# Optimization experiments

Measured on AMD Instinct MI355X. Metric: run time of the kernel, lower is better.

## Reference

```python
import jax, jax.numpy as jnp
import numpy as np

jax.config.update("jax_enable_x64", True)  # torch casts to double for matrix_exp

EPS_DIAG = 1e-6


def setup_inputs() -> dict:
    key = jax.random.key(0)
    B, D, NB, S = 32, 128, 8, 128
    ks = jax.random.split(key, 9)
    return {
        "z0r": jax.random.normal(ks[0], (B, D), jnp.float32),
        "z0i": jax.random.normal(ks[1], (B, D), jnp.float32),
        # uniform grid: dt = time_steps[0] = 0.01, diffs == dt (uniform branch)
        "time_steps": (jnp.arange(S, dtype=jnp.float32) + 1.0) * 0.01,
        "k_coeffs": jax.random.normal(ks[2], (B, NB), jnp.float32),
        "r_coeffs": jax.random.normal(ks[3], (B, NB), jnp.float32),
        "alpha": jax.random.normal(ks[4], (B, 1), jnp.float32),
        "beta": jax.random.normal(ks[5], (B, 1), jnp.float32),
        "K_bases": jax.random.normal(ks[6], (NB, D, D), jnp.float32) * 0.01,
        "R_bases": jax.random.normal(ks[7], (NB, D, D), jnp.float32) * 0.01,
    }


def _build_generator(k_coeffs, r_coeffs, alpha, beta, K_bases, R_bases):
    # A = alpha * skew(K_sum) + beta * -(R_sum^T @ R_sum), per batch element
    K_sum = jnp.einsum("bn,nij->bij", k_coeffs, K_bases)
    R_sum = jnp.einsum("bn,nij->bij", r_coeffs, R_bases)
    skew = K_sum - jnp.swapaxes(K_sum, -1, -2)
    neg_gram = -jnp.einsum("bji,bjk->bik", R_sum, R_sum)  # -(R^T @ R)
    return alpha[..., None] * skew + beta[..., None] * neg_gram  # (B, D, D)


def _propagators(A, time_steps, uniform):
    D = A.shape[-1]
    S = time_steps.shape[0]
    if uniform:
        dt = time_steps[0]
        A64 = A.astype(jnp.float64) * dt.astype(jnp.float64) + EPS_DIAG * jnp.eye(D, dtype=jnp.float64)
        M = jax.vmap(jax.scipy.linalg.expm)(A64).astype(jnp.complex64)  # (B, D, D)
        # cumulative matrix powers M, M^2, ..., M^S via O(log S) associative scan
        Ms = jnp.broadcast_to(M[:, None], (M.shape[0], S, D, D))
        props = jax.lax.associative_scan(jnp.matmul, Ms, axis=1)
    else:
        A_t = A[:, None].astype(jnp.float64) * time_steps.astype(jnp.float64)[None, :, None, None]
        props = jax.vmap(jax.vmap(jax.scipy.linalg.expm))(A_t).astype(jnp.complex64)
    return props  # (B, S, D, D)


def reference(z0r, z0i, time_steps, k_coeffs, r_coeffs, alpha, beta, K_bases, R_bases):
    ts = np.asarray(time_steps)
    uniform = ts.shape[0] <= 1 or np.allclose(ts[1:] - ts[:-1], ts[0], atol=1e-6)
    A = _build_generator(k_coeffs, r_coeffs, alpha, beta, K_bases, R_bases)
    props = _propagators(A, time_steps, uniform)
    z = (z0r + 1j * z0i).astype(jnp.complex64)  # (B, D)
    # z_evolved[b, s, o] = sum_i z[b, i] * props[b, s, o, i]
    return jnp.einsum("bi,bsoi->bso", z, props)
```

## Files before the change

### kernel.cpp

```cpp
#include <hip/hip_runtime.h>

#define BATCH   32
#define DIM     128
#define NBASES  8
#define SSTEPS  128
#define LDA     136

typedef __attribute__((ext_vector_type(8))) short s8v;
typedef __attribute__((ext_vector_type(4))) short s4v;
typedef __attribute__((ext_vector_type(4))) float f4v;

__device__ __forceinline__ f4v mf(s8v a, s8v b, f4v c) {
    return __builtin_amdgcn_mfma_f32_16x16x32_bf16(a, b, c, 0, 0, 0);
}
__device__ __forceinline__ s8v ld8(const short* p) {
    return *reinterpret_cast<const s8v*>(p);
}
__device__ __forceinline__ void st4(short* p, s4v v) {
    *reinterpret_cast<s4v*>(p) = v;
}
__device__ __forceinline__ float upbf(short h) {
    return __uint_as_float(((unsigned)(unsigned short)h) << 16);
}
__device__ __forceinline__ void splitbf(float v, short& hi, short& lo) {
    const unsigned u = __float_as_uint(v);
    hi = (short)(u >> 16);
    const float fh = __uint_as_float(u & 0xffff0000u);
    lo = (short)(__float_as_uint(v - fh) >> 16);
}

__device__ __forceinline__ void write_out(float* __restrict__ outF, int b, int sidx,
                                          int o, int c, float val,
                                          int interleaved, int out_size)
{
    if (interleaved) {
        const int oi = ((b * SSTEPS + sidx) * DIM + o) * 2 + c;
        if (oi < out_size) outF[oi] = val;
    } else if (c == 0) {
        const int oi = (b * SSTEPS + sidx) * DIM + o;
        if (oi < out_size) outF[oi] = val;
    }
}

__device__ __forceinline__ void mm_full(const short* __restrict__ Ah,
                                        const short* __restrict__ Al,
                                        const short* __restrict__ Bh,
                                        const short* __restrict__ Bl,
                                        f4v acc[2][4], int w, int lane)
{
    const int l15 = lane & 15, quad = lane >> 4;
    const int mb = (w & 3) * 32, nb = (w >> 2) * 64;
    #pragma unroll
    for (int kk = 0; kk < DIM; kk += 32) {
        const int ko = kk + quad * 8;
        const s8v a0h = ld8(Ah + (mb +      l15) * LDA + ko);
        const s8v a0l = ld8(Al + (mb +      l15) * LDA + ko);
        const s8v a1h = ld8(Ah + (mb + 16 + l15) * LDA + ko);
        const s8v a1l = ld8(Al + (mb + 16 + l15) * LDA + ko);
        #pragma unroll
        for (int ni = 0; ni < 4; ++ni) {
            const s8v bh = ld8(Bh + (nb + ni * 16 + l15) * LDA + ko);
            const s8v bl = ld8(Bl + (nb + ni * 16 + l15) * LDA + ko);
            acc[0][ni] = mf(a0h, bh, acc[0][ni]);
            acc[0][ni] = mf(a0h, bl, acc[0][ni]);
            acc[0][ni] = mf(a0l, bh, acc[0][ni]);
            acc[1][ni] = mf(a1h, bh, acc[1][ni]);
            acc[1][ni] = mf(a1h, bl, acc[1][ni]);
            acc[1][ni] = mf(a1l, bh, acc[1][ni]);
        }
    }
}

__global__ __launch_bounds__(512, 1)
void htg_mfma(const float* __restrict__ z0r, const float* __restrict__ z0i,
              const float* __restrict__ ts,  const float* __restrict__ kco,
              const float* __restrict__ rco, const float* __restrict__ alp,
              const float* __restrict__ bet, const float* __restrict__ KB,
              const float* __restrict__ RB,  float* __restrict__ outF,
              int interleaved, int out_size)
{
    __shared__ short nm_hi[DIM * LDA], nm_lo[DIM * LDA];
    __shared__ short tr_hi[DIM * LDA], tr_lo[DIM * LDA];
    __shared__ short ht_hi[32 * LDA],  ht_lo[32 * LDA];

    const int b = blockIdx.x, t = threadIdx.x;
    const int w = t >> 6, lane = t & 63;
    const int l15 = lane & 15, quad = lane >> 4;
    const f4v z4 = {0.f, 0.f, 0.f, 0.f};
    const int mb = (w & 3) * 32, nb = (w >> 2) * 64;

    {
        float rc[NBASES], kc[NBASES];
        #pragma unroll
        for (int n = 0; n < NBASES; ++n) {
            rc[n] = rco[b * NBASES + n];
            kc[n] = kco[b * NBASES + n];
        }
        #pragma unroll
        for (int q = 0; q < 8; ++q) {
            const int e = q * 2048 + t * 4;
            float4 r4 = {0.f, 0.f, 0.f, 0.f}, k4 = {0.f, 0.f, 0.f, 0.f};
            #pragma unroll
            for (int n = 0; n < NBASES; ++n) {
                const float4 rv = *reinterpret_cast<const float4*>(RB + n * DIM * DIM + e);
                const float4 kv = *reinterpret_cast<const float4*>(KB + n * DIM * DIM + e);
                r4.x += rc[n] * rv.x; r4.y += rc[n] * rv.y;
                r4.z += rc[n] * rv.z; r4.w += rc[n] * rv.w;
                k4.x += kc[n] * kv.x; k4.y += kc[n] * kv.y;
                k4.z += kc[n] * kv.z; k4.w += kc[n] * kv.w;
            }
            const int r = e >> 7, c = e & 127;
            const float rr[4] = {r4.x, r4.y, r4.z, r4.w};
            const float kk[4] = {k4.x, k4.y, k4.z, k4.w};
            s4v kh, kl;
            #pragma unroll
            for (int j = 0; j < 4; ++j) {
                short hi, lo;
                splitbf(rr[j], hi, lo);
                tr_hi[(c + j) * LDA + r] = hi; tr_lo[(c + j) * LDA + r] = lo;
                splitbf(kk[j], hi, lo);
                kh[j] = hi; kl[j] = lo;
            }
            st4(&nm_hi[r * LDA + c], kh);
            st4(&nm_lo[r * LDA + c], kl);
        }
        if (t < 2 * DIM) {
            const int c = t >> 7, o = t & 127;
            const float zv = (c == 0) ? z0r[b * DIM + o] : z0i[b * DIM + o];
            short hi, lo; splitbf(zv, hi, lo);
            ht_hi[c * LDA + o] = hi; ht_lo[c * LDA + o] = lo;
        }
    }
    __syncthreads();

    f4v acc[2][4];

    #pragma unroll
    for (int i = 0; i < 2; ++i)
        #pragma unroll
        for (int j = 0; j < 4; ++j) acc[i][j] = z4;
    mm_full(tr_hi, tr_lo, tr_hi, tr_lo, acc, w, lane);
    __syncthreads();
    {
        const float alpha = alp[b], beta = bet[b], dtf = ts[0];
        #pragma unroll
        for (int mi = 0; mi < 2; ++mi)
            #pragma unroll
            for (int ni = 0; ni < 4; ++ni)
                #pragma unroll
                for (int r = 0; r < 4; ++r) {
                    const int row = mb + mi * 16 + quad * 4 + r;
                    const int col = nb + ni * 16 + l15;
                    const float k1 = upbf(nm_hi[row * LDA + col]) + upbf(nm_lo[row * LDA + col]);
                    const float k2 = upbf(nm_hi[col * LDA + row]) + upbf(nm_lo[col * LDA + row]);
                    float x = (alpha * (k1 - k2) - beta * acc[mi][ni][r]) * dtf;
                    if (row == col) x += 1e-6f;
                    acc[mi][ni][r] = x;
                }
    }
    __syncthreads();
    #pragma unroll
    for (int mi = 0; mi < 2; ++mi)
        #pragma unroll
        for (int ni = 0; ni < 4; ++ni) {
            const int row0 = mb + mi * 16 + quad * 4;
            const int col  = nb + ni * 16 + l15;
            s4v h4, l4;
            #pragma unroll
            for (int r = 0; r < 4; ++r) {
                short hi, lo;
                splitbf(acc[mi][ni][r], hi, lo);
                nm_hi[(row0 + r) * LDA + col] = hi;
                nm_lo[(row0 + r) * LDA + col] = lo;
                h4[r] = hi; l4[r] = lo;
            }
            st4(&tr_hi[col * LDA + row0], h4);
            st4(&tr_lo[col * LDA + row0], l4);
        }
    __syncthreads();

    float a1v[2][4][4];
    #pragma unroll
    for (int i = 0; i < 2; ++i)
        #pragma unroll
        for (int j = 0; j < 4; ++j) acc[i][j] = z4;
    mm_full(nm_hi, nm_lo, tr_hi, tr_lo, acc, w, lane);
    __syncthreads();
    #pragma unroll
    for (int mi = 0; mi < 2; ++mi)
        #pragma unroll
        for (int ni = 0; ni < 4; ++ni) {
            const int row0 = mb + mi * 16 + quad * 4;
            const int col  = nb + ni * 16 + l15;
            s4v h4, l4;
            #pragma unroll
            for (int r = 0; r < 4; ++r) {
                const int row = row0 + r;
                const float xv = upbf(nm_hi[row * LDA + col]) + upbf(nm_lo[row * LDA + col]);
                const float cv = acc[mi][ni][r];
                a1v[mi][ni][r] = ((row == col) ? 1.f : 0.f) + xv + 0.5f * cv;
                const float a2 = xv * (1.f / 6.f) + cv * (1.f / 24.f);
                short hi, lo;
                splitbf(cv, hi, lo);
                nm_hi[row * LDA + col] = hi;
                nm_lo[row * LDA + col] = lo;
                splitbf(a2, hi, lo);
                h4[r] = hi; l4[r] = lo;
            }
            st4(&tr_hi[col * LDA + row0], h4);
            st4(&tr_lo[col * LDA + row0], l4);
        }
    __syncthreads();

    #pragma unroll
    for (int mi = 0; mi < 2; ++mi)
        #pragma unroll
        for (int ni = 0; ni < 4; ++ni)
            #pragma unroll
            for (int r = 0; r < 4; ++r) acc[mi][ni][r] = a1v[mi][ni][r];
    mm_full(nm_hi, nm_lo, tr_hi, tr_lo, acc, w, lane);
    __syncthreads();
    #pragma unroll
    for (int mi = 0; mi < 2; ++mi)
        #pragma unroll
        for (int ni = 0; ni < 4; ++ni) {
            const int row0 = mb + mi * 16 + quad * 4;
            const int col  = nb + ni * 16 + l15;
            s4v h4, l4;
            #pragma unroll
            for (int r = 0; r < 4; ++r) {
                short hi, lo;
                splitbf(acc[mi][ni][r], hi, lo);
                nm_hi[(row0 + r) * LDA + col] = hi;
                nm_lo[(row0 + r) * LDA + col] = lo;
                h4[r] = hi; l4[r] = lo;
            }
            st4(&tr_hi[col * LDA + row0], h4);
            st4(&tr_lo[col * LDA + row0], l4);
        }
    __syncthreads();

    #pragma unroll
    for (int stage = 0; stage < 4; ++stage) {
        const int J = 1 << stage;
        f4v ar = z4;
        #pragma unroll
        for (int i = 0; i < 2; ++i)
            #pragma unroll
            for (int j = 0; j < 4; ++j) acc[i][j] = z4;
        #pragma unroll
        for (int kk = 0; kk < DIM; kk += 32) {
            const int ko = kk + quad * 8;
            const s8v rah = ld8(nm_hi + (w * 16 + l15) * LDA + ko);
            const s8v ral = ld8(nm_lo + (w * 16 + l15) * LDA + ko);
            const s8v rbh = ld8(ht_hi + l15 * LDA + ko);
            const s8v rbl = ld8(ht_lo + l15 * LDA + ko);
            ar = mf(rah, rbh, ar);
            ar = mf(rah, rbl, ar);
            ar = mf(ral, rbh, ar);
        }
        mm_full(nm_hi, nm_lo, tr_hi, tr_lo, acc, w, lane);
        __syncthreads();
        if (l15 < 2 * J) {
            const int o0 = w * 16 + quad * 4;
            const int sidx = (l15 >> 1) + J - 1;
            s4v h4, l4;
            #pragma unroll
            for (int r = 0; r < 4; ++r) {
                short hi, lo;
                splitbf(ar[r], hi, lo);
                h4[r] = hi; l4[r] = lo;
                write_out(outF, b, sidx, o0 + r, l15 & 1, ar[r], interleaved, out_size);
            }
            st4(&ht_hi[(l15 + 2 * J) * LDA + o0], h4);
            st4(&ht_lo[(l15 + 2 * J) * LDA + o0], l4);
        }
        #pragma unroll
        for (int mi = 0; mi < 2; ++mi)
            #pragma unroll
            for (int ni = 0; ni < 4; ++ni) {
                const int row0 = mb + mi * 16 + quad * 4;
                const int col  = nb + ni * 16 + l15;
                s4v h4, l4;
                #pragma unroll
                for (int r = 0; r < 4; ++r) {
                    short hi, lo;
                    splitbf(acc[mi][ni][r], hi, lo);
                    nm_hi[(row0 + r) * LDA + col] = hi;
                    nm_lo[(row0 + r) * LDA + col] = lo;
                    h4[r] = hi; l4[r] = lo;
                }
                st4(&tr_hi[col * LDA + row0], h4);
                st4(&tr_lo[col * LDA + row0], l4);
            }
        __syncthreads();
    }

    s8v vah[4], val[4];
    #pragma unroll
    for (int k4 = 0; k4 < 4; ++k4) {
        const int ko = k4 * 32 + quad * 8;
        vah[k4] = ld8(nm_hi + (w * 16 + l15) * LDA + ko);
        val[k4] = ld8(nm_lo + (w * 16 + l15) * LDA + ko);
    }
    for (int q = 1; q <= 7; ++q) {
        f4v a2[2] = {z4, z4};
        #pragma unroll
        for (int k4 = 0; k4 < 4; ++k4) {
            const int ko = k4 * 32 + quad * 8;
            #pragma unroll
            for (int ci = 0; ci < 2; ++ci) {
                const s8v bh = ld8(ht_hi + (ci * 16 + l15) * LDA + ko);
                const s8v bl = ld8(ht_lo + (ci * 16 + l15) * LDA + ko);
                a2[ci] = mf(vah[k4], bh, a2[ci]);
                a2[ci] = mf(vah[k4], bl, a2[ci]);
                a2[ci] = mf(val[k4], bh, a2[ci]);
            }
        }
        __syncthreads();
        const int o0 = w * 16 + quad * 4;
        #pragma unroll
        for (int ci = 0; ci < 2; ++ci) {
            const int n = ci * 16 + l15;
            const int sidx = 16 * q + (n >> 1) - 1;
            s4v h4, l4;
            #pragma unroll
            for (int r = 0; r < 4; ++r) {
                short hi, lo;
                splitbf(a2[ci][r], hi, lo);
                h4[r] = hi; l4[r] = lo;
                write_out(outF, b, sidx, o0 + r, n & 1, a2[ci][r], interleaved, out_size);
            }
            if (q < 7 || n < 2) {
                st4(&ht_hi[n * LDA + o0], h4);
                st4(&ht_lo[n * LDA + o0], l4);
            }
        }
        __syncthreads();
    }

    if (t < 2 * DIM) {
        const int c = t >> 7, o = t & 127;
        float a = 0.f;
        #pragma unroll 4
        for (int i = 0; i < DIM; ++i)
            a += (upbf(tr_hi[i * LDA + o]) + upbf(tr_lo[i * LDA + o]))
               * (upbf(ht_hi[c * LDA + i]) + upbf(ht_lo[c * LDA + i]));
        write_out(outF, b, 127, o, c, a, interleaved, out_size);
    }
}

extern "C" void kernel_launch(void* const* d_in, const int* in_sizes, int n_in,
                              void* d_out, int out_size, void* d_ws, size_t ws_size,
                              hipStream_t stream)
{
    (void)in_sizes; (void)n_in; (void)d_ws; (void)ws_size;
    const float* z0r = (const float*)d_in[0];
    const float* z0i = (const float*)d_in[1];
    const float* ts  = (const float*)d_in[2];
    const float* kco = (const float*)d_in[3];
    const float* rco = (const float*)d_in[4];
    const float* alp = (const float*)d_in[5];
    const float* bet = (const float*)d_in[6];
    const float* KB  = (const float*)d_in[7];
    const float* RB  = (const float*)d_in[8];
    float* outF = (float*)d_out;

    const int interleaved = (out_size >= 2 * BATCH * SSTEPS * DIM) ? 1 : 0;

    htg_mfma<<<dim3(BATCH), dim3(512), 0, stream>>>(
        z0r, z0i, ts, kco, rco, alp, bet, KB, RB, outF, interleaved, out_size);
}
```

Before: 122.4 us.

## Double threads per block to 1024 and split matmul tiles across 16 waves

The block grows from 8 to 16 waves. Each wave's 128x128 matmul tile shrinks from 32x64 to 32x32, the z-propagation MFMA stage splits its output columns across wave pairs, and the final dot product is split four ways with a shared-memory reduction. The goal is more latency hiding and more MFMA issue parallelism inside each CU, since only 32 blocks run on a GPU with many more CUs. The cost is that the A-fragment loads are now duplicated across more waves. Barriers also involve more waves, and register pressure is tighter under the 1024-thread launch bound.

```diff
diff --git a/kernel.cpp b/kernel.cpp
--- a/kernel.cpp
+++ b/kernel.cpp
@@ -46,10 +46,9 @@
                                         const short* __restrict__ Al,
                                         const short* __restrict__ Bh,
                                         const short* __restrict__ Bl,
-                                        f4v acc[2][4], int w, int lane)
+                                        f4v acc[2][2], int mb, int nb, int lane)
 {
     const int l15 = lane & 15, quad = lane >> 4;
-    const int mb = (w & 3) * 32, nb = (w >> 2) * 64;
     #pragma unroll
     for (int kk = 0; kk < DIM; kk += 32) {
         const int ko = kk + quad * 8;
@@ -58,7 +57,7 @@
         const s8v a1h = ld8(Ah + (mb + 16 + l15) * LDA + ko);
         const s8v a1l = ld8(Al + (mb + 16 + l15) * LDA + ko);
         #pragma unroll
-        for (int ni = 0; ni < 4; ++ni) {
+        for (int ni = 0; ni < 2; ++ni) {
             const s8v bh = ld8(Bh + (nb + ni * 16 + l15) * LDA + ko);
             const s8v bl = ld8(Bl + (nb + ni * 16 + l15) * LDA + ko);
             acc[0][ni] = mf(a0h, bh, acc[0][ni]);
@@ -71,7 +70,7 @@
     }
 }
 
-__global__ __launch_bounds__(512, 1)
+__global__ __launch_bounds__(1024, 1)
 void htg_mfma(const float* __restrict__ z0r, const float* __restrict__ z0i,
               const float* __restrict__ ts,  const float* __restrict__ kco,
               const float* __restrict__ rco, const float* __restrict__ alp,
@@ -82,12 +81,13 @@
     __shared__ short nm_hi[DIM * LDA], nm_lo[DIM * LDA];
     __shared__ short tr_hi[DIM * LDA], tr_lo[DIM * LDA];
     __shared__ short ht_hi[32 * LDA],  ht_lo[32 * LDA];
+    __shared__ float s_part[1024];
 
     const int b = blockIdx.x, t = threadIdx.x;
     const int w = t >> 6, lane = t & 63;
     const int l15 = lane & 15, quad = lane >> 4;
     const f4v z4 = {0.f, 0.f, 0.f, 0.f};
-    const int mb = (w & 3) * 32, nb = (w >> 2) * 64;
+    const int mb = (w & 3) * 32, nb = (w >> 2) * 32;
 
     {
         float rc[NBASES], kc[NBASES];
@@ -97,8 +97,8 @@
             kc[n] = kco[b * NBASES + n];
         }
         #pragma unroll
-        for (int q = 0; q < 8; ++q) {
-            const int e = q * 2048 + t * 4;
+        for (int q = 0; q < 4; ++q) {
+            const int e = q * 4096 + t * 4;
             float4 r4 = {0.f, 0.f, 0.f, 0.f}, k4 = {0.f, 0.f, 0.f, 0.f};
             #pragma unroll
             for (int n = 0; n < NBASES; ++n) {
@@ -133,20 +133,20 @@
     }
     __syncthreads();
 
-    f4v acc[2][4];
+    f4v acc[2][2];
 
     #pragma unroll
     for (int i = 0; i < 2; ++i)
         #pragma unroll
-        for (int j = 0; j < 4; ++j) acc[i][j] = z4;
-    mm_full(tr_hi, tr_lo, tr_hi, tr_lo, acc, w, lane);
+        for (int j = 0; j < 2; ++j) acc[i][j] = z4;
+    mm_full(tr_hi, tr_lo, tr_hi, tr_lo, acc, mb, nb, lane);
     __syncthreads();
     {
         const float alpha = alp[b], beta = bet[b], dtf = ts[0];
         #pragma unroll
         for (int mi = 0; mi < 2; ++mi)
             #pragma unroll
-            for (int ni = 0; ni < 4; ++ni)
+            for (int ni = 0; ni < 2; ++ni)
                 #pragma unroll
                 for (int r = 0; r < 4; ++r) {
                     const int row = mb + mi * 16 + quad * 4 + r;
@@ -162,7 +162,7 @@
     #pragma unroll
     for (int mi = 0; mi < 2; ++mi)
         #pragma unroll
-        for (int ni = 0; ni < 4; ++ni) {
+        for (int ni = 0; ni < 2; ++ni) {
             const int row0 = mb + mi * 16 + quad * 4;
             const int col  = nb + ni * 16 + l15;
             s4v h4, l4;
@@ -179,17 +179,17 @@
         }
     __syncthreads();
 
-    float a1v[2][4][4];
+    float a1v[2][2][4];
     #pragma unroll
     for (int i = 0; i < 2; ++i)
         #pragma unroll
-        for (int j = 0; j < 4; ++j) acc[i][j] = z4;
-    mm_full(nm_hi, nm_lo, tr_hi, tr_lo, acc, w, lane);
+        for (int j = 0; j < 2; ++j) acc[i][j] = z4;
+    mm_full(nm_hi, nm_lo, tr_hi, tr_lo, acc, mb, nb, lane);
     __syncthreads();
     #pragma unroll
     for (int mi = 0; mi < 2; ++mi)
         #pragma unroll
-        for (int ni = 0; ni < 4; ++ni) {
+        for (int ni = 0; ni < 2; ++ni) {
             const int row0 = mb + mi * 16 + quad * 4;
             const int col  = nb + ni * 16 + l15;
             s4v h4, l4;
@@ -215,15 +215,15 @@
     #pragma unroll
     for (int mi = 0; mi < 2; ++mi)
         #pragma unroll
-        for (int ni = 0; ni < 4; ++ni)
+        for (int ni = 0; ni < 2; ++ni)
             #pragma unroll
             for (int r = 0; r < 4; ++r) acc[mi][ni][r] = a1v[mi][ni][r];
-    mm_full(nm_hi, nm_lo, tr_hi, tr_lo, acc, w, lane);
+    mm_full(nm_hi, nm_lo, tr_hi, tr_lo, acc, mb, nb, lane);
     __syncthreads();
     #pragma unroll
     for (int mi = 0; mi < 2; ++mi)
         #pragma unroll
-        for (int ni = 0; ni < 4; ++ni) {
+        for (int ni = 0; ni < 2; ++ni) {
             const int row0 = mb + mi * 16 + quad * 4;
             const int col  = nb + ni * 16 + l15;
             s4v h4, l4;
@@ -247,21 +247,23 @@
         #pragma unroll
         for (int i = 0; i < 2; ++i)
             #pragma unroll
-            for (int j = 0; j < 4; ++j) acc[i][j] = z4;
-        #pragma unroll
-        for (int kk = 0; kk < DIM; kk += 32) {
-            const int ko = kk + quad * 8;
-            const s8v rah = ld8(nm_hi + (w * 16 + l15) * LDA + ko);
-            const s8v ral = ld8(nm_lo + (w * 16 + l15) * LDA + ko);
-            const s8v rbh = ld8(ht_hi + l15 * LDA + ko);
-            const s8v rbl = ld8(ht_lo + l15 * LDA + ko);
-            ar = mf(rah, rbh, ar);
-            ar = mf(rah, rbl, ar);
-            ar = mf(ral, rbh, ar);
-        }
-        mm_full(nm_hi, nm_lo, tr_hi, tr_lo, acc, w, lane);
+            for (int j = 0; j < 2; ++j) acc[i][j] = z4;
+        if (w < 8) {
+            #pragma unroll
+            for (int kk = 0; kk < DIM; kk += 32) {
+                const int ko = kk + quad * 8;
+                const s8v rah = ld8(nm_hi + (w * 16 + l15) * LDA + ko);
+                const s8v ral = ld8(nm_lo + (w * 16 + l15) * LDA + ko);
+                const s8v rbh = ld8(ht_hi + l15 * LDA + ko);
+                const s8v rbl = ld8(ht_lo + l15 * LDA + ko);
+                ar = mf(rah, rbh, ar);
+                ar = mf(rah, rbl, ar);
+                ar = mf(ral, rbh, ar);
+            }
+        }
+        mm_full(nm_hi, nm_lo, tr_hi, tr_lo, acc, mb, nb, lane);
         __syncthreads();
-        if (l15 < 2 * J) {
+        if (w < 8 && l15 < 2 * J) {
             const int o0 = w * 16 + quad * 4;
             const int sidx = (l15 >> 1) + J - 1;
             s4v h4, l4;
@@ -278,7 +280,7 @@
         #pragma unroll
         for (int mi = 0; mi < 2; ++mi)
             #pragma unroll
-            for (int ni = 0; ni < 4; ++ni) {
+            for (int ni = 0; ni < 2; ++ni) {
                 const int row0 = mb + mi * 16 + quad * 4;
                 const int col  = nb + ni * 16 + l15;
                 s4v h4, l4;
@@ -296,40 +298,37 @@
         __syncthreads();
     }
 
+    const int sw = w >> 1, ct = w & 1;
     s8v vah[4], val[4];
     #pragma unroll
     for (int k4 = 0; k4 < 4; ++k4) {
         const int ko = k4 * 32 + quad * 8;
-        vah[k4] = ld8(nm_hi + (w * 16 + l15) * LDA + ko);
-        val[k4] = ld8(nm_lo + (w * 16 + l15) * LDA + ko);
+        vah[k4] = ld8(nm_hi + (sw * 16 + l15) * LDA + ko);
+        val[k4] = ld8(nm_lo + (sw * 16 + l15) * LDA + ko);
     }
     for (int q = 1; q <= 7; ++q) {
-        f4v a2[2] = {z4, z4};
+        f4v a2 = z4;
         #pragma unroll
         for (int k4 = 0; k4 < 4; ++k4) {
             const int ko = k4 * 32 + quad * 8;
-            #pragma unroll
-            for (int ci = 0; ci < 2; ++ci) {
-                const s8v bh = ld8(ht_hi + (ci * 16 + l15) * LDA + ko);
-                const s8v bl = ld8(ht_lo + (ci * 16 + l15) * LDA + ko);
-                a2[ci] = mf(vah[k4], bh, a2[ci]);
-                a2[ci] = mf(vah[k4], bl, a2[ci]);
-                a2[ci] = mf(val[k4], bh, a2[ci]);
-            }
+            const s8v bh = ld8(ht_hi + (ct * 16 + l15) * LDA + ko);
+            const s8v bl = ld8(ht_lo + (ct * 16 + l15) * LDA + ko);
+            a2 = mf(vah[k4], bh, a2);
+            a2 = mf(vah[k4], bl, a2);
+            a2 = mf(val[k4], bh, a2);
         }
         __syncthreads();
-        const int o0 = w * 16 + quad * 4;
-        #pragma unroll
-        for (int ci = 0; ci < 2; ++ci) {
-            const int n = ci * 16 + l15;
+        {
+            const int o0 = sw * 16 + quad * 4;
+            const int n = ct * 16 + l15;
             const int sidx = 16 * q + (n >> 1) - 1;
             s4v h4, l4;
             #pragma unroll
             for (int r = 0; r < 4; ++r) {
                 short hi, lo;
-                splitbf(a2[ci][r], hi, lo);
-                h4[r] = hi; l4[r] = lo;
-                write_out(outF, b, sidx, o0 + r, n & 1, a2[ci][r], interleaved, out_size);
+                splitbf(a2[r], hi, lo);
+                h4[r] = hi; l4[r] = lo;
+                write_out(outF, b, sidx, o0 + r, n & 1, a2[r], interleaved, out_size);
             }
             if (q < 7 || n < 2) {
                 st4(&ht_hi[n * LDA + o0], h4);
@@ -339,13 +338,20 @@
         __syncthreads();
     }
 
-    if (t < 2 * DIM) {
-        const int c = t >> 7, o = t & 127;
+    {
+        const int o = t & 127, c = (t >> 7) & 1, kq = t >> 8;
+        const int k0 = kq * 32;
         float a = 0.f;
-        #pragma unroll 4
-        for (int i = 0; i < DIM; ++i)
+        #pragma unroll 8
+        for (int i = k0; i < k0 + 32; ++i)
             a += (upbf(tr_hi[i * LDA + o]) + upbf(tr_lo[i * LDA + o]))
                * (upbf(ht_hi[c * LDA + i]) + upbf(ht_lo[c * LDA + i]));
+        s_part[t] = a;
+    }
+    __syncthreads();
+    if (t < 2 * DIM) {
+        const int o = t & 127, c = t >> 7;
+        const float a = s_part[t] + s_part[t + 256] + s_part[t + 512] + s_part[t + 768];
         write_out(outF, b, 127, o, c, a, interleaved, out_size);
     }
 }
@@ -368,6 +374,6 @@
 
     const int interleaved = (out_size >= 2 * BATCH * SSTEPS * DIM) ? 1 : 0;
 
-    htg_mfma<<<dim3(BATCH), dim3(512), 0, stream>>>(
+    htg_mfma<<<dim3(BATCH), dim3(1024), 0, stream>>>(
         z0r, z0i, ts, kco, rco, alp, bet, KB, RB, outF, interleaved, out_size);
 }
```

Measured after the change: 121.7 us. Within noise of the previous version (-0.6%).
